# Kernel optimization log

Measured on AMD Instinct MI355X. Metric: run time of the kernel, lower is better.

## Reference

```python
import jax, jax.numpy as jnp
import numpy as np

N_NODES = 100000
N_MESH_E = 400000
N_WORLD_E = 200000
D = 128


def setup_inputs() -> dict:
    key = jax.random.key(0)
    ks = jax.random.split(key, 12)
    s = lambda fan_in: 1.0 / np.sqrt(fan_in)
    return {
        "x": jax.random.normal(ks[0], (N_NODES, D), jnp.float32),
        "edge_attr": jax.random.normal(ks[1], (N_MESH_E, D), jnp.float32),
        "edge_index": jax.random.randint(ks[2], (2, N_MESH_E), 0, N_NODES, jnp.int64),
        "world_edge_attr": jax.random.normal(ks[3], (N_WORLD_E, D), jnp.float32),
        "world_edge_index": jax.random.randint(ks[4], (2, N_WORLD_E), 0, N_NODES, jnp.int64),
        "W1": jax.random.normal(ks[5], (3 * D, D), jnp.float32) * s(3 * D),
        "b1": jnp.zeros((D,), jnp.float32),
        "W2": jax.random.normal(ks[6], (D, D), jnp.float32) * s(D),
        "b2": jnp.zeros((D,), jnp.float32),
        "W3": jax.random.normal(ks[7], (D, D), jnp.float32) * s(D),
        "b3": jnp.zeros((D,), jnp.float32),
        "ln_gamma": jnp.ones((D,), jnp.float32),
        "ln_beta": jnp.zeros((D,), jnp.float32),
    }


def _layer_norm(h, gamma, beta, eps=1e-5):
    mu = jnp.mean(h, axis=-1, keepdims=True)
    var = jnp.var(h, axis=-1, keepdims=True)
    return (h - mu) * jax.lax.rsqrt(var + eps) * gamma + beta


def reference(x, edge_attr, edge_index, world_edge_attr, world_edge_index,
              W1, b1, W2, b2, W3, b3, ln_gamma, ln_beta):
    num_nodes = x.shape[0]
    # scatter-sum aggregation from mesh edges to receiver nodes
    mesh_recv = edge_index[1]
    mesh_agg = jax.ops.segment_sum(edge_attr, mesh_recv, num_segments=num_nodes)
    # scatter-sum aggregation from world edges
    world_recv = world_edge_index[1]
    world_agg = jax.ops.segment_sum(world_edge_attr, world_recv, num_segments=num_nodes)
    # concat + MLP (2 hidden ReLU layers) + LayerNorm (MeshGraphNets custom_func)
    collected = jnp.concatenate([x, mesh_agg, world_agg], axis=-1)  # [N, 3D]
    h = jax.nn.relu(collected @ W1 + b1)
    h = jax.nn.relu(h @ W2 + b2)
    h = h @ W3 + b3
    out = _layer_norm(h, ln_gamma, ln_beta)
    return out
```

## Files before the change

### kernel.cpp

```cpp
#include <hip/hip_runtime.h>
#include <hip/hip_bf16.h>
#include <stdint.h>

#define NN  100000
#define NME 400000
#define NWE 200000

typedef __bf16 bf16;
typedef __bf16 bf16x8 __attribute__((ext_vector_type(8)));
typedef float  f32x4  __attribute__((ext_vector_type(4)));

static __device__ __forceinline__ bf16 f2bf(float f) {
    union { unsigned int i; float f; } v; v.f = f;
    unsigned int r = (v.i + 0x7fffu + ((v.i >> 16) & 1u)) >> 16;
    union { unsigned short s; bf16 b; } u; u.s = (unsigned short)r;
    return u.b;
}

__global__ void prep_weights(const float* __restrict__ W1, const float* __restrict__ W2,
                             const float* __restrict__ W3, bf16* __restrict__ W1t,
                             bf16* __restrict__ W2t, bf16* __restrict__ W3t) {
    int tid = blockIdx.x * 256 + threadIdx.x;
    if (tid < 49152) {
        int k = tid >> 7, n = tid & 127;
        W1t[n * 384 + k] = f2bf(W1[tid]);
    } else if (tid < 65536) {
        int t2 = tid - 49152;
        int k = t2 >> 7, n = t2 & 127;
        W2t[n * 128 + k] = f2bf(W2[t2]);
    } else if (tid < 81920) {
        int t2 = tid - 65536;
        int k = t2 >> 7, n = t2 & 127;
        W3t[n * 128 + k] = f2bf(W3[t2]);
    }
}

__global__ __launch_bounds__(256) void count_edges(const int* __restrict__ mrecv,
                                                   const int* __restrict__ wrecv,
                                                   int* __restrict__ mdeg,
                                                   int* __restrict__ wdeg) {
    int t = blockIdx.x * 256 + threadIdx.x;
    if (t < NME) {
        atomicAdd(mdeg + mrecv[t], 1);
    } else {
        int t2 = t - NME;
        if (t2 < NWE) atomicAdd(wdeg + wrecv[t2], 1);
    }
}

__global__ __launch_bounds__(256) void scan_part(const int* __restrict__ mdeg,
                                                 const int* __restrict__ wdeg,
                                                 int* __restrict__ bsum) {
    const int nblk = 25;
    int seg = blockIdx.x / nblk;
    int blk = blockIdx.x % nblk;
    const int* deg = (seg == 0) ? mdeg : wdeg;
    const int t = threadIdx.x;
    const int base = blk * 4096;
    int sum = 0;
#pragma unroll
    for (int i = 0; i < 4; ++i) {
        int idx = base + (i * 256 + t) * 4;
        if (idx < NN) {
            int4 v = *(const int4*)(deg + idx);
            sum += v.x + v.y + v.z + v.w;
        }
    }
#pragma unroll
    for (int m = 1; m < 64; m <<= 1) sum += __shfl_xor(sum, m, 64);
    __shared__ int ssum[4];
    if ((t & 63) == 0) ssum[t >> 6] = sum;
    __syncthreads();
    if (t == 0) bsum[blockIdx.x] = ssum[0] + ssum[1] + ssum[2] + ssum[3];
}

__global__ __launch_bounds__(256) void scan_write(int* __restrict__ mdeg, int* __restrict__ wdeg,
                                                  int* __restrict__ mcur, int* __restrict__ wcur,
                                                  const int* __restrict__ bsum) {
    __shared__ int sprefix;
    __shared__ int sscan[256];
    const int nblk = 25;
    int seg = blockIdx.x / nblk;
    int blk = blockIdx.x % nblk;
    int* deg = (seg == 0) ? mdeg : wdeg;
    int* cur = (seg == 0) ? mcur : wcur;
    const int t = threadIdx.x;
    if (t == 0) {
        int s = 0;
        const int* bs = bsum + seg * nblk;
        for (int i = 0; i < blk; ++i) s += bs[i];
        sprefix = s;
    }
    const int base = blk * 4096 + t * 16;
    int v[16];
#pragma unroll
    for (int i = 0; i < 16; i += 4) {
        int idx = base + i;
        if (idx < NN) {
            int4 q = *(const int4*)(deg + idx);
            v[i] = q.x; v[i + 1] = q.y; v[i + 2] = q.z; v[i + 3] = q.w;
        } else {
            v[i] = v[i + 1] = v[i + 2] = v[i + 3] = 0;
        }
    }
    int lsum = 0;
#pragma unroll
    for (int i = 0; i < 16; ++i) lsum += v[i];
    sscan[t] = lsum;
    __syncthreads();
    for (int d = 1; d < 256; d <<= 1) {
        int vv = (t >= d) ? sscan[t - d] : 0;
        __syncthreads();
        sscan[t] += vv;
        __syncthreads();
    }
    int run = sprefix + sscan[t] - lsum;
#pragma unroll
    for (int i = 0; i < 16; i += 4) {
        int idx = base + i;
        if (idx < NN) {
            int4 o;
            o.x = run; run += v[i];
            o.y = run; run += v[i + 1];
            o.z = run; run += v[i + 2];
            o.w = run; run += v[i + 3];
            *(int4*)(deg + idx) = o;
            *(int4*)(cur + idx) = o;
        }
    }
}

__global__ __launch_bounds__(256) void fill_lists(const int* __restrict__ mrecv,
                                                  const int* __restrict__ wrecv,
                                                  int* __restrict__ mcur, int* __restrict__ wcur,
                                                  int* __restrict__ mlist, int* __restrict__ wlist) {
    int t = blockIdx.x * 256 + threadIdx.x;
    if (t < NME) {
        int r = mrecv[t];
        int p = atomicAdd(mcur + r, 1);
        mlist[p] = t;
    } else {
        int t2 = t - NME;
        if (t2 < NWE) {
            int r = wrecv[t2];
            int p = atomicAdd(wcur + r, 1);
            wlist[p] = t2;
        }
    }
}

__global__ __launch_bounds__(256) void gather_sum(const float* __restrict__ attr,
                                                  const int* __restrict__ off,
                                                  const int* __restrict__ list,
                                                  bf16* __restrict__ agg, int nE) {
    int t = blockIdx.x * 256 + threadIdx.x;
    int node = t >> 4;
    int g = t & 15;
    if (node >= NN) return;
    int j0 = off[node];
    int j1 = (node == NN - 1) ? nE : off[node + 1];
    f32x4 lo = (f32x4)0.0f, hi = (f32x4)0.0f;
    for (int j = j0; j < j1; ++j) {
        int e = list[j];
        const float* src = attr + (size_t)e * 128 + g * 8;
        f32x4 a = *(const f32x4*)(src);
        f32x4 b = *(const f32x4*)(src + 4);
        lo += a;
        hi += b;
    }
    bf16x8 o;
#pragma unroll
    for (int i = 0; i < 4; ++i) {
        o[i]     = f2bf(lo[i]);
        o[4 + i] = f2bf(hi[i]);
    }
    *(bf16x8*)(agg + (size_t)node * 128 + g * 8) = o;
}

__global__ __launch_bounds__(256) void node_mlp(
    const float* __restrict__ x, const bf16* __restrict__ magg,
    const bf16* __restrict__ wagg, const bf16* __restrict__ W1t,
    const bf16* __restrict__ W2t, const bf16* __restrict__ W3t,
    const float* __restrict__ b1, const float* __restrict__ b2,
    const float* __restrict__ b3, const float* __restrict__ gam,
    const float* __restrict__ bet, float* __restrict__ out) {
    __shared__ bf16 sh[4 * 32 * 136];
    const int wave = threadIdx.x >> 6;
    const int lane = threadIdx.x & 63;
    const int quad = lane >> 4;
    const int l16 = lane & 15;
    const int node_base = blockIdx.x * 128 + wave * 32;
    bf16* shw = sh + wave * (32 * 136);

    int arow[2];
    arow[0] = node_base + l16;
    arow[1] = node_base + 16 + l16;
    if (arow[0] >= NN) arow[0] = NN - 1;
    if (arow[1] >= NN) arow[1] = NN - 1;

    f32x4 acc[2][8];
#pragma unroll
    for (int rg = 0; rg < 2; ++rg)
#pragma unroll
        for (int t = 0; t < 8; ++t) acc[rg][t] = (f32x4)0.0f;

#pragma unroll
    for (int ks = 0; ks < 12; ++ks) {
        int kg = ks * 32 + quad * 8;
        bf16x8 af[2];
#pragma unroll
        for (int rg = 0; rg < 2; ++rg) {
            if (ks < 4) {
                const float* src = x + (size_t)arow[rg] * 128 + kg;
                f32x4 lo = *(const f32x4*)(src);
                f32x4 hi = *(const f32x4*)(src + 4);
#pragma unroll
                for (int i = 0; i < 4; ++i) {
                    af[rg][i]     = f2bf(lo[i]);
                    af[rg][4 + i] = f2bf(hi[i]);
                }
            } else if (ks < 8) {
                af[rg] = *(const bf16x8*)(magg + (size_t)arow[rg] * 128 + (kg - 128));
            } else {
                af[rg] = *(const bf16x8*)(wagg + (size_t)arow[rg] * 128 + (kg - 256));
            }
        }
#pragma unroll
        for (int t = 0; t < 8; ++t) {
            bf16x8 bfrag = *(const bf16x8*)(W1t + (t * 16 + l16) * 384 + ks * 32 + quad * 8);
            acc[0][t] = __builtin_amdgcn_mfma_f32_16x16x32_bf16(af[0], bfrag, acc[0][t], 0, 0, 0);
            acc[1][t] = __builtin_amdgcn_mfma_f32_16x16x32_bf16(af[1], bfrag, acc[1][t], 0, 0, 0);
        }
    }
#pragma unroll
    for (int t = 0; t < 8; ++t) {
        float bv = b1[t * 16 + l16];
#pragma unroll
        for (int rg = 0; rg < 2; ++rg)
#pragma unroll
            for (int r = 0; r < 4; ++r) {
                float h = acc[rg][t][r] + bv;
                h = h > 0.0f ? h : 0.0f;
                shw[(rg * 16 + quad * 4 + r) * 136 + t * 16 + l16] = f2bf(h);
            }
    }
    __syncthreads();

    bf16x8 a2[2][4];
#pragma unroll
    for (int rg = 0; rg < 2; ++rg)
#pragma unroll
        for (int ks = 0; ks < 4; ++ks)
            a2[rg][ks] = *(const bf16x8*)(shw + (rg * 16 + l16) * 136 + ks * 32 + quad * 8);
#pragma unroll
    for (int rg = 0; rg < 2; ++rg)
#pragma unroll
        for (int t = 0; t < 8; ++t) acc[rg][t] = (f32x4)0.0f;
#pragma unroll
    for (int ks = 0; ks < 4; ++ks) {
#pragma unroll
        for (int t = 0; t < 8; ++t) {
            bf16x8 bfrag = *(const bf16x8*)(W2t + (t * 16 + l16) * 128 + ks * 32 + quad * 8);
            acc[0][t] = __builtin_amdgcn_mfma_f32_16x16x32_bf16(a2[0][ks], bfrag, acc[0][t], 0, 0, 0);
            acc[1][t] = __builtin_amdgcn_mfma_f32_16x16x32_bf16(a2[1][ks], bfrag, acc[1][t], 0, 0, 0);
        }
    }
    __syncthreads();
#pragma unroll
    for (int t = 0; t < 8; ++t) {
        float bv = b2[t * 16 + l16];
#pragma unroll
        for (int rg = 0; rg < 2; ++rg)
#pragma unroll
            for (int r = 0; r < 4; ++r) {
                float h = acc[rg][t][r] + bv;
                h = h > 0.0f ? h : 0.0f;
                shw[(rg * 16 + quad * 4 + r) * 136 + t * 16 + l16] = f2bf(h);
            }
    }
    __syncthreads();

#pragma unroll
    for (int rg = 0; rg < 2; ++rg)
#pragma unroll
        for (int ks = 0; ks < 4; ++ks)
            a2[rg][ks] = *(const bf16x8*)(shw + (rg * 16 + l16) * 136 + ks * 32 + quad * 8);
#pragma unroll
    for (int rg = 0; rg < 2; ++rg)
#pragma unroll
        for (int t = 0; t < 8; ++t) acc[rg][t] = (f32x4)0.0f;
#pragma unroll
    for (int ks = 0; ks < 4; ++ks) {
#pragma unroll
        for (int t = 0; t < 8; ++t) {
            bf16x8 bfrag = *(const bf16x8*)(W3t + (t * 16 + l16) * 128 + ks * 32 + quad * 8);
            acc[0][t] = __builtin_amdgcn_mfma_f32_16x16x32_bf16(a2[0][ks], bfrag, acc[0][t], 0, 0, 0);
            acc[1][t] = __builtin_amdgcn_mfma_f32_16x16x32_bf16(a2[1][ks], bfrag, acc[1][t], 0, 0, 0);
        }
    }
#pragma unroll
    for (int t = 0; t < 8; ++t) {
        float bv = b3[t * 16 + l16];
#pragma unroll
        for (int rg = 0; rg < 2; ++rg)
#pragma unroll
            for (int r = 0; r < 4; ++r) acc[rg][t][r] += bv;
    }

    float gv[8], bv2[8];
#pragma unroll
    for (int t = 0; t < 8; ++t) {
        gv[t]  = gam[t * 16 + l16];
        bv2[t] = bet[t * 16 + l16];
    }
#pragma unroll
    for (int rg = 0; rg < 2; ++rg) {
        float mean[4], rstd[4];
#pragma unroll
        for (int r = 0; r < 4; ++r) {
            float s = 0.0f, s2 = 0.0f;
#pragma unroll
            for (int t = 0; t < 8; ++t) {
                float v = acc[rg][t][r];
                s += v;
                s2 += v * v;
            }
#pragma unroll
            for (int m = 1; m < 16; m <<= 1) {
                s  += __shfl_xor(s, m, 64);
                s2 += __shfl_xor(s2, m, 64);
            }
            float mu = s * (1.0f / 128.0f);
            float var = s2 * (1.0f / 128.0f) - mu * mu;
            mean[r] = mu;
            rstd[r] = rsqrtf(var + 1e-5f);
        }
#pragma unroll
        for (int r = 0; r < 4; ++r) {
            int row = node_base + rg * 16 + quad * 4 + r;
            if (row < NN) {
#pragma unroll
                for (int t = 0; t < 8; ++t) {
                    float o = (acc[rg][t][r] - mean[r]) * rstd[r] * gv[t] + bv2[t];
                    out[(size_t)row * 128 + t * 16 + l16] = o;
                }
            }
        }
    }
}

extern "C" void kernel_launch(void* const* d_in, const int* in_sizes, int n_in,
                              void* d_out, int out_size, void* d_ws, size_t ws_size,
                              hipStream_t stream) {
    const float* x   = (const float*)d_in[0];
    const float* ea  = (const float*)d_in[1];
    const int*   ei  = (const int*)d_in[2];
    const float* wea = (const float*)d_in[3];
    const int*   wei = (const int*)d_in[4];
    const float* W1  = (const float*)d_in[5];
    const float* b1  = (const float*)d_in[6];
    const float* W2  = (const float*)d_in[7];
    const float* b2  = (const float*)d_in[8];
    const float* W3  = (const float*)d_in[9];
    const float* b3  = (const float*)d_in[10];
    const float* gam = (const float*)d_in[11];
    const float* bet = (const float*)d_in[12];

    char* ws = (char*)d_ws;
    bf16* magg = (bf16*)(ws);
    bf16* wagg = (bf16*)(ws + 25600000);
    bf16* W1t  = (bf16*)(ws + 51200000);
    bf16* W2t  = (bf16*)(ws + 51298304);
    bf16* W3t  = (bf16*)(ws + 51331072);
    int*  mdeg = (int*)(ws + 51363840);
    int*  wdeg = (int*)(ws + 51763840);
    int*  mcur = (int*)(ws + 52163840);
    int*  wcur = (int*)(ws + 52563840);
    int*  mlist = (int*)(ws + 52963840);
    int*  wlist = (int*)(ws + 54563840);
    int*  bsum  = (int*)(ws + 55363840);

    hipMemsetAsync(ws + 51363840, 0, 800000, stream);

    prep_weights<<<320, 256, 0, stream>>>(W1, W2, W3, W1t, W2t, W3t);

    count_edges<<<(NME + NWE + 255) / 256, 256, 0, stream>>>(ei + NME, wei + NWE, mdeg, wdeg);
    scan_part<<<50, 256, 0, stream>>>(mdeg, wdeg, bsum);
    scan_write<<<50, 256, 0, stream>>>(mdeg, wdeg, mcur, wcur, bsum);
    fill_lists<<<(NME + NWE + 255) / 256, 256, 0, stream>>>(ei + NME, wei + NWE,
                                                            mcur, wcur, mlist, wlist);

    gather_sum<<<(NN * 16 + 255) / 256, 256, 0, stream>>>(ea, mdeg, mlist, magg, NME);
    gather_sum<<<(NN * 16 + 255) / 256, 256, 0, stream>>>(wea, wdeg, wlist, wagg, NWE);

    node_mlp<<<(NN + 127) / 128, 256, 0, stream>>>(x, magg, wagg, W1t, W2t, W3t,
                                                   b1, b2, b3, gam, bet, (float*)d_out);
}
```

Before: 603.3 us.

## Stage MLP weight slices through double-buffered LDS shared by all waves

```diff
diff --git a/kernel.cpp b/kernel.cpp
--- a/kernel.cpp
+++ b/kernel.cpp
@@ -177,6 +177,17 @@
     *(bf16x8*)(agg + (size_t)node * 128 + g * 8) = o;
 }
 
+static __device__ __forceinline__ const int4* wsrc(const bf16* __restrict__ W1t,
+                                                   const bf16* __restrict__ W2t,
+                                                   const bf16* __restrict__ W3t,
+                                                   int slice, int n, int q) {
+    const bf16* W; int ld, kb;
+    if (slice < 12)      { W = W1t; ld = 384; kb = slice * 32; }
+    else if (slice < 16) { W = W2t; ld = 128; kb = (slice - 12) * 32; }
+    else                 { W = W3t; ld = 128; kb = (slice - 16) * 32; }
+    return (const int4*)(W + n * ld + kb + q * 8);
+}
+
 __global__ __launch_bounds__(256) void node_mlp(
     const float* __restrict__ x, const bf16* __restrict__ magg,
     const bf16* __restrict__ wagg, const bf16* __restrict__ W1t,
@@ -184,13 +195,26 @@
     const float* __restrict__ b1, const float* __restrict__ b2,
     const float* __restrict__ b3, const float* __restrict__ gam,
     const float* __restrict__ bet, float* __restrict__ out) {
-    __shared__ bf16 sh[4 * 32 * 136];
-    const int wave = threadIdx.x >> 6;
-    const int lane = threadIdx.x & 63;
+    __shared__ bf16 sh_w[2][4096];
+    __shared__ bf16 sh_h[4][32 * 136];
+    const int tid  = threadIdx.x;
+    const int wave = tid >> 6;
+    const int lane = tid & 63;
     const int quad = lane >> 4;
-    const int l16 = lane & 15;
+    const int l16  = lane & 15;
     const int node_base = blockIdx.x * 128 + wave * 32;
-    bf16* shw = sh + wave * (32 * 136);
+    bf16* shw = sh_h[wave];
+
+    const int s0 = tid, s1 = tid + 256;
+    const int n0 = ((s0 >> 6) << 4) | (s0 & 15), q0 = (s0 >> 4) & 3;
+    const int n1 = ((s1 >> 6) << 4) | (s1 & 15), q1 = (s1 >> 4) & 3;
+    int4 st0, st1;
+
+    st0 = *wsrc(W1t, W2t, W3t, 0, n0, q0);
+    st1 = *wsrc(W1t, W2t, W3t, 0, n1, q1);
+    *(int4*)(&sh_w[0][s0 * 8]) = st0;
+    *(int4*)(&sh_w[0][s1 * 8]) = st1;
+    __syncthreads();
 
     int arow[2];
     arow[0] = node_base + l16;
@@ -206,6 +230,8 @@
 
 #pragma unroll
     for (int ks = 0; ks < 12; ++ks) {
+        st0 = *wsrc(W1t, W2t, W3t, ks + 1, n0, q0);
+        st1 = *wsrc(W1t, W2t, W3t, ks + 1, n1, q1);
         int kg = ks * 32 + quad * 8;
         bf16x8 af[2];
 #pragma unroll
@@ -225,12 +251,17 @@
                 af[rg] = *(const bf16x8*)(wagg + (size_t)arow[rg] * 128 + (kg - 256));
             }
         }
+        const bf16* wb = sh_w[ks & 1];
 #pragma unroll
         for (int t = 0; t < 8; ++t) {
-            bf16x8 bfrag = *(const bf16x8*)(W1t + (t * 16 + l16) * 384 + ks * 32 + quad * 8);
+            bf16x8 bfrag = *(const bf16x8*)(wb + t * 512 + lane * 8);
             acc[0][t] = __builtin_amdgcn_mfma_f32_16x16x32_bf16(af[0], bfrag, acc[0][t], 0, 0, 0);
             acc[1][t] = __builtin_amdgcn_mfma_f32_16x16x32_bf16(af[1], bfrag, acc[1][t], 0, 0, 0);
         }
+        __syncthreads();
+        *(int4*)(&sh_w[(ks + 1) & 1][s0 * 8]) = st0;
+        *(int4*)(&sh_w[(ks + 1) & 1][s1 * 8]) = st1;
+        __syncthreads();
     }
 #pragma unroll
     for (int t = 0; t < 8; ++t) {
@@ -244,28 +275,30 @@
                 shw[(rg * 16 + quad * 4 + r) * 136 + t * 16 + l16] = f2bf(h);
             }
     }
-    __syncthreads();
-
-    bf16x8 a2[2][4];
+
 #pragma unroll
     for (int rg = 0; rg < 2; ++rg)
 #pragma unroll
-        for (int ks = 0; ks < 4; ++ks)
-            a2[rg][ks] = *(const bf16x8*)(shw + (rg * 16 + l16) * 136 + ks * 32 + quad * 8);
-#pragma unroll
-    for (int rg = 0; rg < 2; ++rg)
-#pragma unroll
         for (int t = 0; t < 8; ++t) acc[rg][t] = (f32x4)0.0f;
 #pragma unroll
     for (int ks = 0; ks < 4; ++ks) {
+        st0 = *wsrc(W1t, W2t, W3t, 13 + ks, n0, q0);
+        st1 = *wsrc(W1t, W2t, W3t, 13 + ks, n1, q1);
+        bf16x8 a2[2];
+        a2[0] = *(const bf16x8*)(shw + l16 * 136 + ks * 32 + quad * 8);
+        a2[1] = *(const bf16x8*)(shw + (16 + l16) * 136 + ks * 32 + quad * 8);
+        const bf16* wb = sh_w[ks & 1];
 #pragma unroll
         for (int t = 0; t < 8; ++t) {
-            bf16x8 bfrag = *(const bf16x8*)(W2t + (t * 16 + l16) * 128 + ks * 32 + quad * 8);
-            acc[0][t] = __builtin_amdgcn_mfma_f32_16x16x32_bf16(a2[0][ks], bfrag, acc[0][t], 0, 0, 0);
-            acc[1][t] = __builtin_amdgcn_mfma_f32_16x16x32_bf16(a2[1][ks], bfrag, acc[1][t], 0, 0, 0);
-        }
-    }
-    __syncthreads();
+            bf16x8 bfrag = *(const bf16x8*)(wb + t * 512 + lane * 8);
+            acc[0][t] = __builtin_amdgcn_mfma_f32_16x16x32_bf16(a2[0], bfrag, acc[0][t], 0, 0, 0);
+            acc[1][t] = __builtin_amdgcn_mfma_f32_16x16x32_bf16(a2[1], bfrag, acc[1][t], 0, 0, 0);
+        }
+        __syncthreads();
+        *(int4*)(&sh_w[(13 + ks) & 1][s0 * 8]) = st0;
+        *(int4*)(&sh_w[(13 + ks) & 1][s1 * 8]) = st1;
+        __syncthreads();
+    }
 #pragma unroll
     for (int t = 0; t < 8; ++t) {
         float bv = b2[t * 16 + l16];
@@ -278,24 +311,32 @@
                 shw[(rg * 16 + quad * 4 + r) * 136 + t * 16 + l16] = f2bf(h);
             }
     }
-    __syncthreads();
 
 #pragma unroll
     for (int rg = 0; rg < 2; ++rg)
 #pragma unroll
-        for (int ks = 0; ks < 4; ++ks)
-            a2[rg][ks] = *(const bf16x8*)(shw + (rg * 16 + l16) * 136 + ks * 32 + quad * 8);
-#pragma unroll
-    for (int rg = 0; rg < 2; ++rg)
-#pragma unroll
         for (int t = 0; t < 8; ++t) acc[rg][t] = (f32x4)0.0f;
 #pragma unroll
     for (int ks = 0; ks < 4; ++ks) {
+        if (ks < 3) {
+            st0 = *wsrc(W1t, W2t, W3t, 17 + ks, n0, q0);
+            st1 = *wsrc(W1t, W2t, W3t, 17 + ks, n1, q1);
+        }
+        bf16x8 a2[2];
+        a2[0] = *(const bf16x8*)(shw + l16 * 136 + ks * 32 + quad * 8);
+        a2[1] = *(const bf16x8*)(shw + (16 + l16) * 136 + ks * 32 + quad * 8);
+        const bf16* wb = sh_w[ks & 1];
 #pragma unroll
         for (int t = 0; t < 8; ++t) {
-            bf16x8 bfrag = *(const bf16x8*)(W3t + (t * 16 + l16) * 128 + ks * 32 + quad * 8);
-            acc[0][t] = __builtin_amdgcn_mfma_f32_16x16x32_bf16(a2[0][ks], bfrag, acc[0][t], 0, 0, 0);
-            acc[1][t] = __builtin_amdgcn_mfma_f32_16x16x32_bf16(a2[1][ks], bfrag, acc[1][t], 0, 0, 0);
+            bf16x8 bfrag = *(const bf16x8*)(wb + t * 512 + lane * 8);
+            acc[0][t] = __builtin_amdgcn_mfma_f32_16x16x32_bf16(a2[0], bfrag, acc[0][t], 0, 0, 0);
+            acc[1][t] = __builtin_amdgcn_mfma_f32_16x16x32_bf16(a2[1], bfrag, acc[1][t], 0, 0, 0);
+        }
+        if (ks < 3) {
+            __syncthreads();
+            *(int4*)(&sh_w[(17 + ks) & 1][s0 * 8]) = st0;
+            *(int4*)(&sh_w[(17 + ks) & 1][s1 * 8]) = st1;
+            __syncthreads();
         }
     }
 #pragma unroll
```

After: 539.0 us. 10.6% less time.
